# Kernel optimization log

Hardware: AMD Instinct MI355X
Metric: run time of the kernel (lower is better)

Reference implementation:

```python
import jax, jax.numpy as jnp
import numpy as np

D_MODEL = 1024
N_HEADS = 16
D_HEAD = D_MODEL // N_HEADS
B, S = 2, 2048


def setup_inputs() -> dict:
    key = jax.random.key(0)
    ks = jax.random.split(key, 14)
    std = 0.02
    inp = {
        "query": jax.random.normal(ks[0], (B, S, D_MODEL), dtype=jnp.float32),
        "key": jax.random.normal(ks[1], (B, S, D_MODEL), dtype=jnp.float32),
        "value": jax.random.normal(ks[2], (B, S, D_MODEL), dtype=jnp.float32),
        "mask": jax.random.randint(ks[3], (B, 1, S, S), 0, 2, dtype=jnp.int32),
        "position_bias": jax.random.normal(ks[4], (1, N_HEADS, S, S), dtype=jnp.float32),
        "w_q": jax.random.normal(ks[5], (D_MODEL, D_MODEL), dtype=jnp.float32) * std,
        "b_q": jnp.zeros((D_MODEL,), dtype=jnp.float32),
        "w_k": jax.random.normal(ks[6], (D_MODEL, D_MODEL), dtype=jnp.float32) * std,
        "b_k": jnp.zeros((D_MODEL,), dtype=jnp.float32),
        "w_v": jax.random.normal(ks[7], (D_MODEL, D_MODEL), dtype=jnp.float32) * std,
        "b_v": jnp.zeros((D_MODEL,), dtype=jnp.float32),
        "w_o": jax.random.normal(ks[8], (D_MODEL, D_MODEL), dtype=jnp.float32) * std,
        "b_o": jnp.zeros((D_MODEL,), dtype=jnp.float32),
    }
    return inp


def reference(query, key, value, mask, position_bias,
              w_q, b_q, w_k, b_k, w_v, b_v, w_o, b_o):
    b = query.shape[0]
    # projections: torch Linear computes x @ W^T + b
    def proj(x, w, bias):
        y = x @ w.T + bias                       # [b, s, D]
        return y.reshape(b, -1, N_HEADS, D_HEAD).transpose(0, 2, 1, 3)  # [b, h, s, d]

    Q = proj(query, w_q, b_q)
    K = proj(key, w_k, b_k)
    V = proj(value, w_v, b_v)

    scale = 1.0 / jnp.sqrt(jnp.asarray(D_HEAD, dtype=Q.dtype))
    scores = jnp.einsum("bhqd,bhkd->bhqk", Q, K) * scale
    scores = scores + position_bias
    scores = jnp.where(mask == 0, jnp.asarray(-1e9, dtype=scores.dtype), scores)
    attn = jax.nn.softmax(scores, axis=-1)       # dropout is identity at eval
    ctx = jnp.einsum("bhqk,bhkd->bhqd", attn, V)  # [b, h, s, d]
    ctx = ctx.transpose(0, 2, 1, 3).reshape(b, -1, N_HEADS * D_HEAD)
    return ctx @ w_o.T + b_o
```

## Files before the change

kernel.cpp:

```cpp
#include <hip/hip_runtime.h>
#include <hip/hip_bf16.h>

#define S_LEN 2048
#define DM 1024
#define NH 16
#define DH 64
#define MTOK 4096

typedef __attribute__((ext_vector_type(8))) __bf16 bf16x8;
typedef __attribute__((ext_vector_type(4))) float f32x4;
typedef __attribute__((ext_vector_type(16))) float f32x16;
typedef unsigned short u16;
typedef unsigned long long u64;

__device__ __forceinline__ u16 f2bf(float f) {
  union { float f; unsigned u; } a; a.f = f;
  unsigned u = a.u;
  u += 0x7fffu + ((u >> 16) & 1u);
  return (u16)(u >> 16);
}

__device__ __forceinline__ bf16x8 ld_bf8(const u16* p) {
  return *reinterpret_cast<const bf16x8*>(p);
}

__global__ void k_convert(const float* __restrict__ src, u16* __restrict__ dst, int n4) {
  int i = blockIdx.x * blockDim.x + threadIdx.x;
  int stride = gridDim.x * blockDim.x;
  for (; i < n4; i += stride) {
    float4 v = reinterpret_cast<const float4*>(src)[i];
    ushort4 o;
    o.x = f2bf(v.x); o.y = f2bf(v.y); o.z = f2bf(v.z); o.w = f2bf(v.w);
    reinterpret_cast<ushort4*>(dst)[i] = o;
  }
}

__global__ void k_maskpack(const int* __restrict__ m, u64* __restrict__ o, int n) {
  int i = blockIdx.x * blockDim.x + threadIdx.x;
  int stride = gridDim.x * blockDim.x;
  for (; i < n; i += stride) {
    u64 bal = __ballot(m[i] != 0);
    if ((i & 63) == 0) o[i >> 6] = bal;
  }
}

template<int MODE>
__global__ __launch_bounds__(256) void k_gemm(
    const u16* __restrict__ A, const u16* __restrict__ Bw,
    const float* __restrict__ bias, void* __restrict__ dst) {
  constexpr int K = DM;
  __shared__ u16 As[128 * 32];
  __shared__ u16 Bs[128 * 32];
  const int tid = threadIdx.x;
  const int lane = tid & 63;
  const int wid = tid >> 6;
  const int wm = wid >> 1, wn = wid & 1;
  const int bm = blockIdx.x * 128;
  const int bn = blockIdx.y * 128;
  const int r0 = tid >> 2;
  const int c0 = (tid & 3) * 8;
  const int fr = lane & 15;
  const int fk = (lane >> 4) * 8;

  f32x4 acc[4][4] = {};

  const u16* ga = A + (size_t)(bm + r0) * K + c0;
  const u16* gb = Bw + (size_t)(bn + r0) * K + c0;

  for (int kt = 0; kt < K; kt += 32) {
    __syncthreads();
    __builtin_amdgcn_global_load_lds(
        (const __attribute__((address_space(1))) void*)(ga + kt),
        (__attribute__((address_space(3))) void*)(&As[r0 * 32 + c0]), 16, 0, 0);
    __builtin_amdgcn_global_load_lds(
        (const __attribute__((address_space(1))) void*)(ga + (size_t)64 * K + kt),
        (__attribute__((address_space(3))) void*)(&As[(r0 + 64) * 32 + c0]), 16, 0, 0);
    __builtin_amdgcn_global_load_lds(
        (const __attribute__((address_space(1))) void*)(gb + kt),
        (__attribute__((address_space(3))) void*)(&Bs[r0 * 32 + c0]), 16, 0, 0);
    __builtin_amdgcn_global_load_lds(
        (const __attribute__((address_space(1))) void*)(gb + (size_t)64 * K + kt),
        (__attribute__((address_space(3))) void*)(&Bs[(r0 + 64) * 32 + c0]), 16, 0, 0);
    __syncthreads();
    bf16x8 af[4], bfr[4];
#pragma unroll
    for (int m = 0; m < 4; ++m) af[m] = ld_bf8(&As[(wm * 64 + m * 16 + fr) * 32 + fk]);
#pragma unroll
    for (int n = 0; n < 4; ++n) bfr[n] = ld_bf8(&Bs[(wn * 64 + n * 16 + fr) * 32 + fk]);
#pragma unroll
    for (int m = 0; m < 4; ++m)
#pragma unroll
      for (int n = 0; n < 4; ++n)
        acc[m][n] = __builtin_amdgcn_mfma_f32_16x16x32_bf16(af[m], bfr[n], acc[m][n], 0, 0, 0);
  }

  const int cr = (lane >> 4) * 4;
  const int cc = lane & 15;
#pragma unroll
  for (int m = 0; m < 4; ++m) {
#pragma unroll
    for (int n = 0; n < 4; ++n) {
      const int colg = bn + wn * 64 + n * 16 + cc;
      const float bv = bias[colg];
      const int rbase = bm + wm * 64 + m * 16 + cr;
      if (MODE == 2) {
        float* o = (float*)dst;
#pragma unroll
        for (int r = 0; r < 4; ++r)
          o[(size_t)(rbase + r) * DM + colg] = acc[m][n][r] + bv;
      } else if (MODE == 0) {
        u16* o = (u16*)dst;
        const int h = colg >> 6, d = colg & 63;
#pragma unroll
        for (int r = 0; r < 4; ++r) {
          const int tok = rbase + r;
          const int b = tok >> 11, s = tok & 2047;
          o[(((size_t)(b * NH + h) * S_LEN) + s) * DH + d] = f2bf(acc[m][n][r] + bv);
        }
      } else {
        u16* o = (u16*)dst;
        const int h = colg >> 6, d = colg & 63;
        const int tok = rbase;
        const int b = tok >> 11, s = tok & 2047;
        ushort4 pk;
        pk.x = f2bf(acc[m][n][0] + bv);
        pk.y = f2bf(acc[m][n][1] + bv);
        pk.z = f2bf(acc[m][n][2] + bv);
        pk.w = f2bf(acc[m][n][3] + bv);
        *reinterpret_cast<ushort4*>(&o[(((size_t)(b * NH + h) * DH) + d) * S_LEN + s]) = pk;
      }
    }
  }
}

__global__ __launch_bounds__(256, 2) void k_attn(
    const u16* __restrict__ Qb, const u16* __restrict__ Kb, const u16* __restrict__ Vt,
    const float* __restrict__ bias, const u64* __restrict__ mpk,
    u16* __restrict__ ctx) {
  __shared__ u16 lds[2][4][4096];
  const int tid = threadIdx.x;
  const int lane = tid & 63;
  const int w = tid >> 6;
  const int b = w >> 1;
  const int h = blockIdx.y;
  const int q0 = blockIdx.x * 64 + (w & 1) * 32;
  const int lq = lane & 31;
  const int hi = lane >> 5;

  const float* bp = bias + (size_t)h * S_LEN * S_LEN;

  bf16x8 qf[4];
  f32x16 cacc[2] = {};
  float m_run = -1e30f, l_run = 0.f;
  {
    const u16* Qp = Qb + (size_t)(b * NH + h) * S_LEN * DH;
#pragma unroll
    for (int d0 = 0; d0 < 4; ++d0)
      qf[d0] = ld_bf8(&Qp[(size_t)(q0 + lq) * DH + d0 * 16 + hi * 8]);
  }

#define STAGE(ktv, cb) {                                                          \
    _Pragma("unroll") for (int i = 0; i < 2; ++i) {                               \
      const int el = (i * 256 + tid) * 8;                                         \
      const int rr = el >> 6;                                                     \
      const int ce = ((tid & 7) * 8) ^ ((rr & 7) << 3);                           \
      _Pragma("unroll") for (int b2 = 0; b2 < 2; ++b2) {                          \
        const u16* ksrc = Kb + (size_t)(b2 * NH + h) * S_LEN * DH                 \
                          + (size_t)((ktv) + rr) * DH + ce;                       \
        const u16* vsrc = Vt + (size_t)(b2 * NH + h) * DH * S_LEN                 \
                          + (size_t)rr * S_LEN + (ktv) + ce;                      \
        __builtin_amdgcn_global_load_lds(                                         \
            (const __attribute__((address_space(1))) void*)ksrc,                  \
            (__attribute__((address_space(3))) void*)&lds[cb][b2][el], 16, 0, 0); \
        __builtin_amdgcn_global_load_lds(                                         \
            (const __attribute__((address_space(1))) void*)vsrc,                  \
            (__attribute__((address_space(3))) void*)&lds[cb][2 + b2][el], 16, 0, 0); \
      } } }

#define LDSREAD(cb, tile, row, cel) \
    ld_bf8(&lds[cb][tile][(row) * 64 + (((cel)) ^ (((row) & 7) << 3))])

#define LOADB(BV, ktv) {                                                          \
    _Pragma("unroll") for (int kb = 0; kb < 2; ++kb)                              \
      _Pragma("unroll") for (int rq = 0; rq < 4; ++rq)                            \
        BV[kb][rq] = *reinterpret_cast<const float4*>(                            \
            &bp[(size_t)(q0 + lq) * S_LEN + (ktv) + kb * 32 + rq * 8 + hi * 4]); }

#define BARRIER() {                                                               \
    asm volatile("s_waitcnt vmcnt(9) lgkmcnt(0)" ::: "memory");                   \
    __builtin_amdgcn_sched_barrier(0);                                            \
    __builtin_amdgcn_s_barrier();                                                 \
    __builtin_amdgcn_sched_barrier(0); }

#define BODY(T, BV, MW, BVN, MWN) {                                               \
    const int ktv = (T) * 64;                                                     \
    BARRIER();                                                                    \
    if ((T) + 1 < S_LEN / 64) {                                                   \
      STAGE(ktv + 64, c ^ 1);                                                     \
      __builtin_amdgcn_sched_barrier(0);                                          \
      LOADB(BVN, ktv + 64);                                                       \
      MWN = mpk[((size_t)(b * S_LEN + q0 + lq)) * 32 + (ktv >> 6) + 1];           \
    }                                                                             \
    f32x16 sc0 = {}, sc1 = {};                                                    \
    __builtin_amdgcn_s_setprio(1);                                                \
    _Pragma("unroll") for (int d0 = 0; d0 < 4; ++d0) {                            \
      bf16x8 ka0 = LDSREAD(c, b, lq, d0 * 16 + hi * 8);                           \
      sc0 = __builtin_amdgcn_mfma_f32_32x32x16_bf16(ka0, qf[d0], sc0, 0, 0, 0);   \
      bf16x8 ka1 = LDSREAD(c, b, 32 + lq, d0 * 16 + hi * 8);                      \
      sc1 = __builtin_amdgcn_mfma_f32_32x32x16_bf16(ka1, qf[d0], sc1, 0, 0, 0);   \
    }                                                                             \
    __builtin_amdgcn_s_setprio(0);                                                \
    _Pragma("unroll") for (int r = 0; r < 16; ++r) {                              \
      const int cr_ = (r & 3) + 8 * (r >> 2);                                     \
      const float v0_ = sc0[r] * 0.125f + ((const float*)&BV[0][r >> 2])[r & 3];  \
      sc0[r] = ((MW >> (cr_ + 4 * hi)) & 1) ? v0_ : -1e9f;                        \
      const float v1_ = sc1[r] * 0.125f + ((const float*)&BV[1][r >> 2])[r & 3];  \
      sc1[r] = ((MW >> (32 + cr_ + 4 * hi)) & 1) ? v1_ : -1e9f;                   \
    }                                                                             \
    float vm = fmaxf(sc0[0], sc1[0]);                                             \
    _Pragma("unroll") for (int r = 1; r < 16; ++r)                                \
      vm = fmaxf(vm, fmaxf(sc0[r], sc1[r]));                                      \
    vm = fmaxf(vm, __shfl_xor(vm, 32));                                           \
    if (!__all(vm <= m_run)) {                                                    \
      const float mn = fmaxf(m_run, vm);                                          \
      const float corr = __expf(m_run - mn);                                      \
      m_run = mn;                                                                 \
      l_run *= corr;                                                              \
      _Pragma("unroll") for (int r = 0; r < 16; ++r) {                            \
        cacc[0][r] *= corr; cacc[1][r] *= corr; }                                 \
    }                                                                             \
    float ssum = 0.f;                                                             \
    _Pragma("unroll") for (int r = 0; r < 16; ++r) {                              \
      const float p0 = __expf(sc0[r] - m_run); sc0[r] = p0;                       \
      const float p1 = __expf(sc1[r] - m_run); sc1[r] = p1;                       \
      ssum += p0 + p1;                                                            \
    }                                                                             \
    ssum += __shfl_xor(ssum, 32);                                                 \
    l_run += ssum;                                                                \
    unsigned pw0[8], pw1[8];                                                      \
    _Pragma("unroll") for (int i2 = 0; i2 < 8; ++i2) {                            \
      pw0[i2] = (unsigned)f2bf(sc0[2 * i2]) | ((unsigned)f2bf(sc0[2 * i2 + 1]) << 16); \
      pw1[i2] = (unsigned)f2bf(sc1[2 * i2]) | ((unsigned)f2bf(sc1[2 * i2 + 1]) << 16); \
    }                                                                             \
    bf16x8 pf[4];                                                                 \
    _Pragma("unroll") for (int kb = 0; kb < 2; ++kb)                              \
      _Pragma("unroll") for (int ch = 0; ch < 2; ++ch) {                          \
        const unsigned a0 = kb ? pw1[ch * 4 + 0] : pw0[ch * 4 + 0];               \
        const unsigned a1 = kb ? pw1[ch * 4 + 1] : pw0[ch * 4 + 1];               \
        const unsigned a2 = kb ? pw1[ch * 4 + 2] : pw0[ch * 4 + 2];               \
        const unsigned a3 = kb ? pw1[ch * 4 + 3] : pw0[ch * 4 + 3];               \
        const unsigned sx0 = __shfl_xor(a0, 32), sx1 = __shfl_xor(a1, 32);        \
        const unsigned sx2 = __shfl_xor(a2, 32), sx3 = __shfl_xor(a3, 32);        \
        union { unsigned u[4]; bf16x8 v; } f;                                     \
        f.u[0] = hi ? sx2 : a0;                                                   \
        f.u[1] = hi ? sx3 : a1;                                                   \
        f.u[2] = hi ? a2 : sx0;                                                   \
        f.u[3] = hi ? a3 : sx1;                                                   \
        pf[kb * 2 + ch] = f.v;                                                    \
      }                                                                           \
    __builtin_amdgcn_s_setprio(1);                                                \
    _Pragma("unroll") for (int db = 0; db < 2; ++db)                              \
      _Pragma("unroll") for (int kc = 0; kc < 4; ++kc) {                          \
        bf16x8 va = LDSREAD(c, 2 + b, db * 32 + lq, kc * 16 + hi * 8);            \
        cacc[db] = __builtin_amdgcn_mfma_f32_32x32x16_bf16(va, pf[kc], cacc[db], 0, 0, 0); \
      }                                                                           \
    __builtin_amdgcn_s_setprio(0);                                                \
    c ^= 1;                                                                       \
  }

  float4 bvA[2][4], bvB[2][4];
  u64 mwA, mwB;
  STAGE(0, 0);
  __builtin_amdgcn_sched_barrier(0);
  LOADB(bvA, 0);
  mwA = mpk[((size_t)(b * S_LEN + q0 + lq)) * 32];
  int c = 0;
  for (int t0 = 0; t0 < S_LEN / 64; t0 += 2) {
    BODY(t0, bvA, mwA, bvB, mwB);
    BODY(t0 + 1, bvB, mwB, bvA, mwA);
  }
#undef STAGE
#undef LDSREAD
#undef LOADB
#undef BARRIER
#undef BODY

  {
    const float linv = 1.0f / l_run;
    u16* cp = ctx + ((size_t)(b * S_LEN + q0 + lq)) * DM + h * DH;
#pragma unroll
    for (int db = 0; db < 2; ++db)
#pragma unroll
      for (int r = 0; r < 16; ++r)
        cp[db * 32 + (r & 3) + 8 * (r >> 2) + 4 * hi] = f2bf(cacc[db][r] * linv);
  }
}

extern "C" void kernel_launch(void* const* d_in, const int* in_sizes, int n_in,
                              void* d_out, int out_size, void* d_ws, size_t ws_size,
                              hipStream_t stream) {
  const float* q   = (const float*)d_in[0];
  const float* k   = (const float*)d_in[1];
  const float* v   = (const float*)d_in[2];
  const int*   msk = (const int*)d_in[3];
  const float* pb  = (const float*)d_in[4];
  const float* w_q = (const float*)d_in[5];
  const float* b_q = (const float*)d_in[6];
  const float* w_k = (const float*)d_in[7];
  const float* b_k = (const float*)d_in[8];
  const float* w_v = (const float*)d_in[9];
  const float* b_v = (const float*)d_in[10];
  const float* w_o = (const float*)d_in[11];
  const float* b_o = (const float*)d_in[12];
  float* out = (float*)d_out;

  char* ws = (char*)d_ws;
  u16* wq_bf = (u16*)(ws + ((size_t)0 << 20));
  u16* wk_bf = (u16*)(ws + ((size_t)2 << 20));
  u16* wv_bf = (u16*)(ws + ((size_t)4 << 20));
  u16* wo_bf = (u16*)(ws + ((size_t)6 << 20));
  u16* x_bf  = (u16*)(ws + ((size_t)8 << 20));
  u16* Qb    = (u16*)(ws + ((size_t)16 << 20));
  u16* Kb    = (u16*)(ws + ((size_t)24 << 20));
  u16* Vtb   = (u16*)(ws + ((size_t)32 << 20));
  u64* mpk   = (u64*)(ws + ((size_t)40 << 20));

  dim3 blk(256);
  const int n4w = DM * DM / 4;
  const int n4x = MTOK * DM / 4;
  k_convert<<<dim3(1024), blk, 0, stream>>>(w_q, wq_bf, n4w);
  k_convert<<<dim3(1024), blk, 0, stream>>>(w_k, wk_bf, n4w);
  k_convert<<<dim3(1024), blk, 0, stream>>>(w_v, wv_bf, n4w);
  k_convert<<<dim3(1024), blk, 0, stream>>>(w_o, wo_bf, n4w);
  k_maskpack<<<dim3(2048), blk, 0, stream>>>(msk, mpk, 2 * S_LEN * S_LEN);

  dim3 gg(32, 8);
  k_convert<<<dim3(2048), blk, 0, stream>>>(q, x_bf, n4x);
  k_gemm<0><<<gg, blk, 0, stream>>>(x_bf, wq_bf, b_q, Qb);
  k_convert<<<dim3(2048), blk, 0, stream>>>(k, x_bf, n4x);
  k_gemm<0><<<gg, blk, 0, stream>>>(x_bf, wk_bf, b_k, Kb);
  k_convert<<<dim3(2048), blk, 0, stream>>>(v, x_bf, n4x);
  k_gemm<1><<<gg, blk, 0, stream>>>(x_bf, wv_bf, b_v, Vtb);

  k_attn<<<dim3(32, NH), blk, 0, stream>>>(Qb, Kb, Vtb, pb, mpk, x_bf);
  k_gemm<2><<<gg, blk, 0, stream>>>(x_bf, wo_bf, b_o, out);
}
```

Baseline: 283.7 us.

## Give each attention block one batch with four query waves sharing K/V tiles

Each attention block now covers a single batch (grid z) and 128 queries, one 32-query slice per wave, instead of two batches with two waves each. All four waves read the same K/V tile, so LDS per stage is halved and the launch bound allows 4 blocks per CU. The row max and row sum reductions become tree reductions, which shortens the dependency chains. The trade-off is that the 2048x2048 bias tile per head is now fetched separately by each batch's blocks rather than being shared inside one block, which may raise bias traffic. The higher occupancy target may also squeeze the register budget.

```diff
diff --git a/kernel.cpp b/kernel.cpp
--- a/kernel.cpp
+++ b/kernel.cpp
@@ -133,21 +133,23 @@
   }
 }
 
-__global__ __launch_bounds__(256, 2) void k_attn(
+__global__ __launch_bounds__(256, 4) void k_attn(
     const u16* __restrict__ Qb, const u16* __restrict__ Kb, const u16* __restrict__ Vt,
     const float* __restrict__ bias, const u64* __restrict__ mpk,
     u16* __restrict__ ctx) {
-  __shared__ u16 lds[2][4][4096];
+  __shared__ u16 lds[2][2][4096];
   const int tid = threadIdx.x;
   const int lane = tid & 63;
   const int w = tid >> 6;
-  const int b = w >> 1;
+  const int b = blockIdx.z;
   const int h = blockIdx.y;
-  const int q0 = blockIdx.x * 64 + (w & 1) * 32;
+  const int q0 = blockIdx.x * 128 + w * 32;
   const int lq = lane & 31;
   const int hi = lane >> 5;
 
   const float* bp = bias + (size_t)h * S_LEN * S_LEN;
+  const u16* Kp = Kb + (size_t)(b * NH + h) * S_LEN * DH;
+  const u16* Vp = Vt + (size_t)(b * NH + h) * DH * S_LEN;
 
   bf16x8 qf[4];
   f32x16 cacc[2] = {};
@@ -164,18 +166,15 @@
       const int el = (i * 256 + tid) * 8;                                         \
       const int rr = el >> 6;                                                     \
       const int ce = ((tid & 7) * 8) ^ ((rr & 7) << 3);                           \
-      _Pragma("unroll") for (int b2 = 0; b2 < 2; ++b2) {                          \
-        const u16* ksrc = Kb + (size_t)(b2 * NH + h) * S_LEN * DH                 \
-                          + (size_t)((ktv) + rr) * DH + ce;                       \
-        const u16* vsrc = Vt + (size_t)(b2 * NH + h) * DH * S_LEN                 \
-                          + (size_t)rr * S_LEN + (ktv) + ce;                      \
-        __builtin_amdgcn_global_load_lds(                                         \
-            (const __attribute__((address_space(1))) void*)ksrc,                  \
-            (__attribute__((address_space(3))) void*)&lds[cb][b2][el], 16, 0, 0); \
-        __builtin_amdgcn_global_load_lds(                                         \
-            (const __attribute__((address_space(1))) void*)vsrc,                  \
-            (__attribute__((address_space(3))) void*)&lds[cb][2 + b2][el], 16, 0, 0); \
-      } } }
+      const u16* ksrc = Kp + (size_t)((ktv) + rr) * DH + ce;                      \
+      const u16* vsrc = Vp + (size_t)rr * S_LEN + (ktv) + ce;                     \
+      __builtin_amdgcn_global_load_lds(                                           \
+          (const __attribute__((address_space(1))) void*)ksrc,                    \
+          (__attribute__((address_space(3))) void*)&lds[cb][0][el], 16, 0, 0);    \
+      __builtin_amdgcn_global_load_lds(                                           \
+          (const __attribute__((address_space(1))) void*)vsrc,                    \
+          (__attribute__((address_space(3))) void*)&lds[cb][1][el], 16, 0, 0);    \
+    } }
 
 #define LDSREAD(cb, tile, row, cel) \
     ld_bf8(&lds[cb][tile][(row) * 64 + (((cel)) ^ (((row) & 7) << 3))])
@@ -204,9 +203,9 @@
     f32x16 sc0 = {}, sc1 = {};                                                    \
     __builtin_amdgcn_s_setprio(1);                                                \
     _Pragma("unroll") for (int d0 = 0; d0 < 4; ++d0) {                            \
-      bf16x8 ka0 = LDSREAD(c, b, lq, d0 * 16 + hi * 8);                           \
+      bf16x8 ka0 = LDSREAD(c, 0, lq, d0 * 16 + hi * 8);                           \
       sc0 = __builtin_amdgcn_mfma_f32_32x32x16_bf16(ka0, qf[d0], sc0, 0, 0, 0);   \
-      bf16x8 ka1 = LDSREAD(c, b, 32 + lq, d0 * 16 + hi * 8);                      \
+      bf16x8 ka1 = LDSREAD(c, 0, 32 + lq, d0 * 16 + hi * 8);                      \
       sc1 = __builtin_amdgcn_mfma_f32_32x32x16_bf16(ka1, qf[d0], sc1, 0, 0, 0);   \
     }                                                                             \
     __builtin_amdgcn_s_setprio(0);                                                \
@@ -217,9 +216,11 @@
       const float v1_ = sc1[r] * 0.125f + ((const float*)&BV[1][r >> 2])[r & 3];  \
       sc1[r] = ((MW >> (32 + cr_ + 4 * hi)) & 1) ? v1_ : -1e9f;                   \
     }                                                                             \
-    float vm = fmaxf(sc0[0], sc1[0]);                                             \
-    _Pragma("unroll") for (int r = 1; r < 16; ++r)                                \
-      vm = fmaxf(vm, fmaxf(sc0[r], sc1[r]));                                      \
+    float mt[16];                                                                 \
+    _Pragma("unroll") for (int r = 0; r < 16; ++r) mt[r] = fmaxf(sc0[r], sc1[r]); \
+    _Pragma("unroll") for (int r = 0; r < 8; ++r) mt[r] = fmaxf(mt[r], mt[r + 8]);\
+    _Pragma("unroll") for (int r = 0; r < 4; ++r) mt[r] = fmaxf(mt[r], mt[r + 4]);\
+    float vm = fmaxf(fmaxf(mt[0], mt[1]), fmaxf(mt[2], mt[3]));                   \
     vm = fmaxf(vm, __shfl_xor(vm, 32));                                           \
     if (!__all(vm <= m_run)) {                                                    \
       const float mn = fmaxf(m_run, vm);                                          \
@@ -229,12 +230,15 @@
       _Pragma("unroll") for (int r = 0; r < 16; ++r) {                            \
         cacc[0][r] *= corr; cacc[1][r] *= corr; }                                 \
     }                                                                             \
-    float ssum = 0.f;                                                             \
+    float st[16];                                                                 \
     _Pragma("unroll") for (int r = 0; r < 16; ++r) {                              \
       const float p0 = __expf(sc0[r] - m_run); sc0[r] = p0;                       \
       const float p1 = __expf(sc1[r] - m_run); sc1[r] = p1;                       \
-      ssum += p0 + p1;                                                            \
-    }                                                                             \
+      st[r] = p0 + p1;                                                            \
+    }                                                                             \
+    _Pragma("unroll") for (int r = 0; r < 8; ++r) st[r] += st[r + 8];             \
+    _Pragma("unroll") for (int r = 0; r < 4; ++r) st[r] += st[r + 4];             \
+    float ssum = (st[0] + st[1]) + (st[2] + st[3]);                               \
     ssum += __shfl_xor(ssum, 32);                                                 \
     l_run += ssum;                                                                \
     unsigned pw0[8], pw1[8];                                                      \
@@ -261,7 +265,7 @@
     __builtin_amdgcn_s_setprio(1);                                                \
     _Pragma("unroll") for (int db = 0; db < 2; ++db)                              \
       _Pragma("unroll") for (int kc = 0; kc < 4; ++kc) {                          \
-        bf16x8 va = LDSREAD(c, 2 + b, db * 32 + lq, kc * 16 + hi * 8);            \
+        bf16x8 va = LDSREAD(c, 1, db * 32 + lq, kc * 16 + hi * 8);                \
         cacc[db] = __builtin_amdgcn_mfma_f32_32x32x16_bf16(va, pf[kc], cacc[db], 0, 0, 0); \
       }                                                                           \
     __builtin_amdgcn_s_setprio(0);                                                \
@@ -342,6 +346,6 @@
   k_convert<<<dim3(2048), blk, 0, stream>>>(v, x_bf, n4x);
   k_gemm<1><<<gg, blk, 0, stream>>>(x_bf, wv_bf, b_v, Vtb);
 
-  k_attn<<<dim3(32, NH), blk, 0, stream>>>(Qb, Kb, Vtb, pb, mpk, x_bf);
+  k_attn<<<dim3(16, NH, 2), blk, 0, stream>>>(Qb, Kb, Vtb, pb, mpk, x_bf);
   k_gemm<2><<<gg, blk, 0, stream>>>(x_bf, wo_bf, b_o, out);
 }
```

Result: slower. 631.1 us (+122.5%).
